# Performance work log

Measured on AMD Instinct MI355X. Metric: run time of the kernel, lower is better.

Reference implementation:

```python
import jax, jax.numpy as jnp
import numpy as np

C, P, PQ, D, B, HW = 32, 64, 4, 2048, 256, 7
N = HW * HW  # 49 spatial positions


def _bn(x, g, b):
    # eval-mode BatchNorm2d with running_mean=0, running_var=1
    s = g / jnp.sqrt(1.0 + 1e-5)
    return x * s[None, :, None, None] + b[None, :, None, None]


def _g1x1(x, w):
    # grouped 1x1 conv: x [B, C*pin, H, W], w [C, pout, pin]
    Bs, _, Hh, Ww = x.shape
    xg = x.reshape(Bs, C, w.shape[2], Hh, Ww)
    y = jnp.einsum('bcihw,coi->bcohw', xg, w)
    return y.reshape(Bs, C * w.shape[1], Hh, Ww)


def setup_inputs() -> dict:
    key = jax.random.key(0)
    ks = iter(jax.random.split(key, 40))
    def rn(shape, s=1.0):
        return jax.random.normal(next(ks), shape, jnp.float32) * s
    inp = {
        'x': rn((B, D, HW, HW)),
        'W1': rn((C * P, D), 0.02), 'g1': 1.0 + rn((C * P,), 0.1), 'b1': rn((C * P,), 0.1),
        'W2': rn((C * P, P, 3, 3), 0.04), 'g2': 1.0 + rn((C * P,), 0.1), 'b2': rn((C * P,), 0.1),
        'Wq': rn((C, PQ, P), 0.1), 'gq': 1.0 + rn((C * PQ,), 0.1), 'bq': rn((C * PQ,), 0.1),
        'Wk': rn((C, PQ, P), 0.1), 'gk': 1.0 + rn((C * PQ,), 0.1), 'bk': rn((C * PQ,), 0.1),
        'Wout': rn((C, PQ, P), 0.1), 'gout': 1.0 + rn((C * PQ,), 0.1), 'bout': rn((C * PQ,), 0.1),
        'Wcr': rn((C, C, PQ), 0.1), 'gcr': 1.0 + rn((C * C,), 0.1), 'bcr': rn((C * C,), 0.1),
        'gcr1': 1.0 + rn((C * PQ,), 0.1), 'bcr1': rn((C * PQ,), 0.1),
        'Wa': rn((C, P, PQ), 0.1), 'ba': rn((C * P,), 0.1),
        'Wb': rn((C, P, PQ), 0.1), 'bb': rn((C * P,), 0.1),
        'W3': rn((D, C * P), 0.02), 'g3': 1.0 + rn((D,), 0.1), 'b3': rn((D,), 0.1),
    }
    return inp


def reference(x, W1, g1, b1, W2, g2, b2, Wq, gq, bq, Wk, gk, bk,
              Wout, gout, bout, Wcr, gcr, bcr, gcr1, bcr1,
              Wa, ba, Wb, bb, W3, g3, b3):
    # stem: 1x1 conv + BN, grouped 3x3 conv + BN
    Xc = _bn(jnp.einsum('bdhw,ed->behw', x, W1), g1, b1)             # [B,2048,7,7]
    Zc = _bn(jax.lax.conv_general_dilated(
        Xc, W2, (1, 1), 'SAME', feature_group_count=C,
        dimension_numbers=('NCHW', 'OIHW', 'NCHW')), g2, b2)         # [B,2048,7,7]

    # channel self-attention: per-group q(1xp_) @ k(p_xN)
    pooled = jnp.mean(Zc, axis=(2, 3), keepdims=True)                # AvgPool2d(7) -> 1x1
    q = _bn(_g1x1(pooled, Wq), gq, bq).reshape(-1, C, PQ)            # [B,c,p_]
    k = _bn(_g1x1(Zc, Wk), gk, bk).reshape(-1, C, PQ, N)             # [B,c,p_,N]
    scores = jnp.einsum('bcp,bcpn->bcn', q, k)                       # [B,c,N]
    # torch Softmax2d on 3D [B,1,N] normalizes dim -3 == batch dim (faithful quirk)
    M = jax.nn.softmax(scores, axis=0)                               # [B,c,N]

    Zg = Zc.reshape(-1, C, P, N)
    zout = jnp.einsum('bcpn,bcn->bcp', Zg, M).reshape(-1, C * P, 1, 1)
    hc = _bn(_g1x1(zout, Wout), gout, bout)                          # [B,128,1,1]

    # channel-relation: A [B,c,c] mixes H [B,c,p_]
    A = jnp.tanh(_bn(_g1x1(hc, Wcr), gcr, bcr)).reshape(-1, C, C)
    A = jnp.swapaxes(A, 1, 2)                                        # chunk/cat transpose
    Hm = hc.reshape(-1, C, PQ)                                       # [B,c,p_]
    mix = jnp.matmul(A, Hm) + Hm                                     # [B,c,p_]
    hc_ = jax.nn.relu(_bn(mix.reshape(-1, C * PQ, 1, 1), gcr1, bcr1)).reshape(-1, C, PQ)

    # broadcast back to spatial via attention maps
    M_ = M / jnp.max(M)
    Mchc = jnp.einsum('bcp,bcn->bcpn', hc_, M_).reshape(-1, C * PQ, HW, HW)

    alpha = _g1x1(Mchc, Wa) + ba[None, :, None, None]                # [B,2048,7,7]
    beta = _g1x1(Mchc, Wb) + bb[None, :, None, None]
    Xc_ = jax.nn.relu(Zc * alpha + beta)
    cm = Zc * Xc_

    OUT = _bn(jnp.einsum('behw,de->bdhw', cm, W3), g3, b3)
    return OUT + x
```

## Files before the change

### kernel.cpp

```cpp
#include <hip/hip_runtime.h>
#include <hip/hip_bf16.h>
#include <stdint.h>

#define DI __device__ __forceinline__

typedef __attribute__((ext_vector_type(8))) short short8;
typedef __attribute__((ext_vector_type(4))) float floatx4;

DI float bf2f(short u) {
  union { unsigned int i; float f; } v;
  v.i = ((unsigned int)(unsigned short)u) << 16;
  return v.f;
}
DI short f2bf(float f) {
  union { float f; unsigned int i; } v; v.f = f;
  unsigned int r = v.i + 0x7FFFu + ((v.i >> 16) & 1u);
  return (short)(r >> 16);
}

DI void gload16(const void* g, void* l) {
  __builtin_amdgcn_global_load_lds(
      (const __attribute__((address_space(1))) void*)g,
      (__attribute__((address_space(3))) void*)l,
      16, 0, 0);
}

__global__ __launch_bounds__(256) void k_cvt(const float* __restrict__ src,
                                             short* __restrict__ dst, int n) {
  int i = blockIdx.x * 256 + threadIdx.x;
  if (i < n) dst[i] = f2bf(src[i]);
}

__global__ __launch_bounds__(256) void k_w2r(const float* __restrict__ W2,
                                             short* __restrict__ W2R) {
  int idx = blockIdx.x * 256 + threadIdx.x;
  if (idx >= 32 * 9 * 64 * 64) return;
  int pi = idx & 63;
  int po = (idx >> 6) & 63;
  int ct = idx >> 12;
  int tap = ct % 9, c = ct / 9;
  W2R[idx] = f2bf(W2[((c * 64 + po) * 64 + pi) * 9 + tap]);
}

__global__ __launch_bounds__(256) void k_xt(const float* __restrict__ x,
                                            short* __restrict__ xT) {
  __shared__ float tile[64 * 49];
  int b = blockIdx.x, dc = blockIdx.y;
  const float* xp = x + ((size_t)b * 2048 + dc * 64) * 49;
  for (int i = threadIdx.x; i < 64 * 49; i += 256) tile[i] = xp[i];
  __syncthreads();
  for (int i = threadIdx.x; i < 64 * 49; i += 256) {
    int n = i >> 6, dl = i & 63;
    xT[((size_t)(b * 49 + n)) * 2048 + dc * 64 + dl] = f2bf(tile[dl * 49 + n]);
  }
}

__global__ __launch_bounds__(512, 4) void k_gemm1(
    const short* __restrict__ xT, const short* __restrict__ W1b,
    const float* __restrict__ g1, const float* __restrict__ b1,
    short* __restrict__ XcPad) {
  __shared__ __attribute__((aligned(16))) short As[4096];
  __shared__ __attribute__((aligned(16))) short Bs[4096];
  const int tid = threadIdx.x;
  const int wave = tid >> 6, lane = tid & 63;
  const int wg = blockIdx.x;
  const int swz = (wg & 7) * 196 + (wg >> 3);
  const int mt = swz >> 4, et = swz & 15;
  const int srow = tid >> 2, schunk = tid & 3;
  const short* asrc = xT + (size_t)(mt * 128 + srow) * 2048 + schunk * 8;
  const short* bsrc = W1b + (size_t)(et * 128 + srow) * 2048 + schunk * 8;
  short* alds = &As[wave * 512];
  short* blds = &Bs[wave * 512];
  const int wr = wave >> 2, wc = wave & 3;
  const int aoff = (wr * 64 + (lane & 15)) * 32 + (lane >> 4) * 8;
  const int boff = (wc * 32 + (lane & 15)) * 32 + (lane >> 4) * 8;
  floatx4 acc[4][2] = {};
#pragma unroll 1
  for (int kt = 0; kt < 64; ++kt) {
    const int ko = kt * 32;
    gload16(asrc + ko, alds);
    gload16(bsrc + ko, blds);
    __syncthreads();
    short8 a[4], b[2];
#pragma unroll
    for (int i = 0; i < 4; ++i) a[i] = *(const short8*)&As[aoff + i * 512];
#pragma unroll
    for (int j = 0; j < 2; ++j) b[j] = *(const short8*)&Bs[boff + j * 512];
#pragma unroll
    for (int i = 0; i < 4; ++i)
#pragma unroll
      for (int j = 0; j < 2; ++j)
        acc[i][j] = __builtin_amdgcn_mfma_f32_16x16x32_bf16(a[i], b[j], acc[i][j], 0, 0, 0);
    __syncthreads();
  }
  const float rs = rsqrtf(1.0f + 1e-5f);
  size_t abase[16];
#pragma unroll
  for (int i = 0; i < 4; ++i)
#pragma unroll
    for (int r = 0; r < 4; ++r) {
      int m = mt * 128 + wr * 64 + i * 16 + (lane >> 4) * 4 + r;
      int bb = m / 49, n = m % 49, h = n / 7, w = n % 7;
      abase[i * 4 + r] = ((size_t)bb * 81 + (h + 1) * 9 + (w + 1)) * 2048;
    }
#pragma unroll
  for (int j = 0; j < 2; ++j) {
    int e = et * 128 + wc * 32 + j * 16 + (lane & 15);
    float s = g1[e] * rs, bo = b1[e];
#pragma unroll
    for (int i = 0; i < 4; ++i)
#pragma unroll
      for (int r = 0; r < 4; ++r)
        XcPad[abase[i * 4 + r] + e] = f2bf(acc[i][j][r] * s + bo);
  }
}

__global__ __launch_bounds__(512, 4) void k_conv(
    const short* __restrict__ XcPad, const short* __restrict__ W2R,
    const float* __restrict__ g2, const float* __restrict__ b2,
    short* __restrict__ ZcT) {
  __shared__ __attribute__((aligned(16))) short As[4096];
  __shared__ __attribute__((aligned(16))) short Bs[2048];
  const int tid = threadIdx.x;
  const int wave = tid >> 6, lane = tid & 63;
  const int wg = blockIdx.x;
  const int swz = (wg & 7) * 392 + (wg >> 3);
  const int mt = swz >> 5, c = swz & 31;
  const int srow = tid >> 2, schunk = tid & 3;
  int m0 = mt * 128 + srow;
  int b0 = m0 / 49, n0 = m0 % 49, h0 = n0 / 7, w0 = n0 % 7;
  const short* abase = XcPad + (size_t)c * 64 + schunk * 8;
  const short* wbase = W2R + (size_t)c * 9 * 4096 + srow * 64 + schunk * 8;
  short* alds = &As[wave * 512];
  short* blds = &Bs[wave * 512];
  const int wr = wave >> 1, wc = wave & 1;
  const int aoff = (wr * 32 + (lane & 15)) * 32 + (lane >> 4) * 8;
  const int boff = (wc * 32 + (lane & 15)) * 32 + (lane >> 4) * 8;
  floatx4 acc[2][2] = {};
#pragma unroll 1
  for (int tap = 0; tap < 9; ++tap) {
    const int dy = tap / 3, dx = tap % 3;
    const size_t r0 = ((size_t)b0 * 81 + (h0 + dy) * 9 + (w0 + dx)) * 2048;
#pragma unroll
    for (int kk = 0; kk < 2; ++kk) {
      gload16(abase + r0 + kk * 32, alds);
      if (wave < 4) gload16(wbase + tap * 4096 + kk * 32, blds);
      __syncthreads();
      short8 a[2], b[2];
#pragma unroll
      for (int i = 0; i < 2; ++i) a[i] = *(const short8*)&As[aoff + i * 512];
#pragma unroll
      for (int j = 0; j < 2; ++j) b[j] = *(const short8*)&Bs[boff + j * 512];
#pragma unroll
      for (int i = 0; i < 2; ++i)
#pragma unroll
        for (int j = 0; j < 2; ++j)
          acc[i][j] = __builtin_amdgcn_mfma_f32_16x16x32_bf16(a[i], b[j], acc[i][j], 0, 0, 0);
      __syncthreads();
    }
  }
  const float rs = rsqrtf(1.0f + 1e-5f);
#pragma unroll
  for (int j = 0; j < 2; ++j) {
    int e = c * 64 + wc * 32 + j * 16 + (lane & 15);
    float s = g2[e] * rs, bo = b2[e];
#pragma unroll
    for (int i = 0; i < 2; ++i)
#pragma unroll
      for (int r = 0; r < 4; ++r) {
        int m = mt * 128 + wr * 32 + i * 16 + (lane >> 4) * 4 + r;
        ZcT[(size_t)m * 2048 + e] = f2bf(acc[i][j][r] * s + bo);
      }
  }
}

__global__ __launch_bounds__(256) void k_scores(
    const short* __restrict__ ZcT, const float* __restrict__ Wq,
    const float* __restrict__ gq, const float* __restrict__ bq,
    const float* __restrict__ Wk, const float* __restrict__ gk,
    const float* __restrict__ bk, float* __restrict__ scores) {
  int b = blockIdx.x, t = threadIdx.x;
  __shared__ float pooled[2048];
  __shared__ float qv[128];
  const float rs = rsqrtf(1.0f + 1e-5f);
  for (int e = t; e < 2048; e += 256) {
    float s = 0.f;
    for (int n = 0; n < 49; ++n) s += bf2f(ZcT[((size_t)(b * 49 + n)) * 2048 + e]);
    pooled[e] = s * (1.0f / 49.0f);
  }
  __syncthreads();
  if (t < 128) {
    int c = t >> 2;
    float s = 0.f;
    for (int pi = 0; pi < 64; ++pi) s += Wq[t * 64 + pi] * pooled[c * 64 + pi];
    qv[t] = s * gq[t] * rs + bq[t];
  }
  __syncthreads();
  for (int idx = t; idx < 1568; idx += 256) {
    int c = idx / 49, n = idx % 49;
    const short8* z = (const short8*)&ZcT[((size_t)(b * 49 + n)) * 2048 + c * 64];
    float acc[4] = {0.f, 0.f, 0.f, 0.f};
#pragma unroll
    for (int p8 = 0; p8 < 8; ++p8) {
      short8 v = z[p8];
#pragma unroll
      for (int j = 0; j < 8; ++j) {
        float zv = bf2f(v[j]);
#pragma unroll
        for (int pq = 0; pq < 4; ++pq)
          acc[pq] += Wk[(c * 4 + pq) * 64 + p8 * 8 + j] * zv;
      }
    }
    float sc = 0.f;
#pragma unroll
    for (int pq = 0; pq < 4; ++pq) {
      float kv = acc[pq] * gk[c * 4 + pq] * rs + bk[c * 4 + pq];
      sc += qv[c * 4 + pq] * kv;
    }
    scores[b * 1568 + idx] = sc;
  }
}

__global__ __launch_bounds__(256) void k_softmax(const float* __restrict__ scores,
                                                 float* __restrict__ Msm,
                                                 unsigned int* __restrict__ maxM) {
  int cn = blockIdx.x, t = threadIdx.x;
  float v = scores[t * 1568 + cn];
  __shared__ float red[4], red2[4];
  float m = v;
#pragma unroll
  for (int o = 1; o < 64; o <<= 1) m = fmaxf(m, __shfl_xor(m, o));
  if ((t & 63) == 0) red[t >> 6] = m;
  __syncthreads();
  m = fmaxf(fmaxf(red[0], red[1]), fmaxf(red[2], red[3]));
  float e = expf(v - m);
  float s = e;
#pragma unroll
  for (int o = 1; o < 64; o <<= 1) s += __shfl_xor(s, o);
  if ((t & 63) == 0) red2[t >> 6] = s;
  __syncthreads();
  s = red2[0] + red2[1] + red2[2] + red2[3];
  Msm[t * 1568 + cn] = e / s;
  if (t == 0) atomicMax(maxM, __float_as_uint(1.0f / s));
}

__global__ __launch_bounds__(256) void k_tail(
    const short* __restrict__ ZcT, const float* __restrict__ Msm,
    const float* __restrict__ Wout, const float* __restrict__ gout,
    const float* __restrict__ bout, const float* __restrict__ Wcr,
    const float* __restrict__ gcr, const float* __restrict__ bcr,
    const float* __restrict__ gcr1, const float* __restrict__ bcr1,
    const float* __restrict__ Wa, const float* __restrict__ Wb,
    float* __restrict__ va, float* __restrict__ vb) {
  int b = blockIdx.x, t = threadIdx.x;
  __shared__ float Mrow[1568];
  __shared__ float zout[2048];
  __shared__ float hcl[128];
  __shared__ float tb[1024];
  __shared__ float hcp[128];
  const float rs = rsqrtf(1.0f + 1e-5f);
  for (int i = t; i < 1568; i += 256) Mrow[i] = Msm[b * 1568 + i];
  __syncthreads();
  for (int e = t; e < 2048; e += 256) {
    int c = e >> 6;
    float s = 0.f;
    for (int n = 0; n < 49; ++n)
      s += bf2f(ZcT[((size_t)(b * 49 + n)) * 2048 + e]) * Mrow[c * 49 + n];
    zout[e] = s;
  }
  __syncthreads();
  if (t < 128) {
    int c = t >> 2;
    float s = 0.f;
    for (int p = 0; p < 64; ++p) s += Wout[t * 64 + p] * zout[c * 64 + p];
    hcl[t] = s * gout[t] * rs + bout[t];
  }
  __syncthreads();
  for (int i = t; i < 1024; i += 256) {
    int c = i >> 5;
    float s = 0.f;
#pragma unroll
    for (int k = 0; k < 4; ++k) s += Wcr[i * 4 + k] * hcl[c * 4 + k];
    tb[i] = tanhf(s * gcr[i] * rs + bcr[i]);
  }
  __syncthreads();
  if (t < 128) {
    int i = t >> 2, pq = t & 3;
    float s = hcl[t];
    for (int j = 0; j < 32; ++j) s += tb[j * 32 + i] * hcl[j * 4 + pq];
    hcp[t] = fmaxf(s * gcr1[t] * rs + bcr1[t], 0.0f);
  }
  __syncthreads();
  for (int e = t; e < 2048; e += 256) {
    int c = e >> 6;
    float sa = 0.f, sb = 0.f;
#pragma unroll
    for (int pq = 0; pq < 4; ++pq) {
      float h = hcp[c * 4 + pq];
      sa += Wa[e * 4 + pq] * h;
      sb += Wb[e * 4 + pq] * h;
    }
    va[b * 2048 + e] = sa;
    vb[b * 2048 + e] = sb;
  }
}

__global__ __launch_bounds__(256) void k_cm(
    const short* __restrict__ ZcT, const float* __restrict__ Msm,
    const unsigned int* __restrict__ maxM, const float* __restrict__ va,
    const float* __restrict__ vb, const float* __restrict__ ba,
    const float* __restrict__ bb, short* __restrict__ cm) {
  int m = blockIdx.x;
  int b = m / 49, n = m % 49;
  __shared__ float Minv[32];
  if (threadIdx.x < 32) {
    float mx = __uint_as_float(*maxM);
    Minv[threadIdx.x] = Msm[b * 1568 + threadIdx.x * 49 + n] / mx;
  }
  __syncthreads();
  const int e0 = threadIdx.x * 8;
  short8 z8 = *(const short8*)&ZcT[(size_t)m * 2048 + e0];
  const float mi = Minv[e0 >> 6];
  short8 o;
#pragma unroll
  for (int j = 0; j < 8; ++j) {
    float zc = bf2f(z8[j]);
    float al = va[b * 2048 + e0 + j] * mi + ba[e0 + j];
    float bt = vb[b * 2048 + e0 + j] * mi + bb[e0 + j];
    float xc = fmaxf(zc * al + bt, 0.0f);
    o[j] = f2bf(zc * xc);
  }
  *(short8*)&cm[(size_t)m * 2048 + e0] = o;
}

__global__ __launch_bounds__(512, 4) void k_gemm2(
    const short* __restrict__ W3b, const short* __restrict__ cm,
    const float* __restrict__ g3, const float* __restrict__ b3,
    const float* __restrict__ x, float* __restrict__ out) {
  __shared__ __attribute__((aligned(16))) short As[4096];
  __shared__ __attribute__((aligned(16))) short Bs[4096];
  const int tid = threadIdx.x;
  const int wave = tid >> 6, lane = tid & 63;
  const int wg = blockIdx.x;
  const int swz = (wg & 7) * 196 + (wg >> 3);
  const int mt = swz >> 4, dt = swz & 15;
  const int srow = tid >> 2, schunk = tid & 3;
  const short* asrc = W3b + (size_t)(dt * 128 + srow) * 2048 + schunk * 8;
  const short* bsrc = cm + (size_t)(mt * 128 + srow) * 2048 + schunk * 8;
  short* alds = &As[wave * 512];
  short* blds = &Bs[wave * 512];
  const int wr = wave >> 2, wc = wave & 3;
  const int aoff = (wr * 64 + (lane & 15)) * 32 + (lane >> 4) * 8;
  const int boff = (wc * 32 + (lane & 15)) * 32 + (lane >> 4) * 8;
  floatx4 acc[4][2] = {};
#pragma unroll 1
  for (int kt = 0; kt < 64; ++kt) {
    const int ko = kt * 32;
    gload16(asrc + ko, alds);
    gload16(bsrc + ko, blds);
    __syncthreads();
    short8 a[4], b[2];
#pragma unroll
    for (int i = 0; i < 4; ++i) a[i] = *(const short8*)&As[aoff + i * 512];
#pragma unroll
    for (int j = 0; j < 2; ++j) b[j] = *(const short8*)&Bs[boff + j * 512];
#pragma unroll
    for (int i = 0; i < 4; ++i)
#pragma unroll
      for (int j = 0; j < 2; ++j)
        acc[i][j] = __builtin_amdgcn_mfma_f32_16x16x32_bf16(a[i], b[j], acc[i][j], 0, 0, 0);
    __syncthreads();
  }
  const float rs = rsqrtf(1.0f + 1e-5f);
  size_t cbb[2];
#pragma unroll
  for (int j = 0; j < 2; ++j) {
    int m = mt * 128 + wc * 32 + j * 16 + (lane & 15);
    int bb = m / 49, n = m % 49;
    cbb[j] = (size_t)bb * (2048 * 49) + n;
  }
#pragma unroll
  for (int i = 0; i < 4; ++i)
#pragma unroll
    for (int r = 0; r < 4; ++r) {
      int d = dt * 128 + wr * 64 + i * 16 + (lane >> 4) * 4 + r;
      float s = g3[d] * rs, bo = b3[d];
      size_t dterm = (size_t)d * 49;
#pragma unroll
      for (int j = 0; j < 2; ++j) {
        size_t adr = cbb[j] + dterm;
        out[adr] = acc[i][j][r] * s + bo + x[adr];
      }
    }
}

extern "C" void kernel_launch(void* const* d_in, const int* in_sizes, int n_in,
                              void* d_out, int out_size, void* d_ws, size_t ws_size,
                              hipStream_t stream) {
  (void)in_sizes; (void)n_in; (void)out_size; (void)ws_size;
  const float* x    = (const float*)d_in[0];
  const float* W1   = (const float*)d_in[1];
  const float* g1   = (const float*)d_in[2];
  const float* b1   = (const float*)d_in[3];
  const float* W2   = (const float*)d_in[4];
  const float* g2   = (const float*)d_in[5];
  const float* b2   = (const float*)d_in[6];
  const float* Wq   = (const float*)d_in[7];
  const float* gq   = (const float*)d_in[8];
  const float* bq   = (const float*)d_in[9];
  const float* Wk   = (const float*)d_in[10];
  const float* gk   = (const float*)d_in[11];
  const float* bk   = (const float*)d_in[12];
  const float* Wout = (const float*)d_in[13];
  const float* gout = (const float*)d_in[14];
  const float* bout = (const float*)d_in[15];
  const float* Wcr  = (const float*)d_in[16];
  const float* gcr  = (const float*)d_in[17];
  const float* bcr  = (const float*)d_in[18];
  const float* gcr1 = (const float*)d_in[19];
  const float* bcr1 = (const float*)d_in[20];
  const float* Wa   = (const float*)d_in[21];
  const float* ba   = (const float*)d_in[22];
  const float* Wb   = (const float*)d_in[23];
  const float* bb   = (const float*)d_in[24];
  const float* W3   = (const float*)d_in[25];
  const float* g3   = (const float*)d_in[26];
  const float* b3   = (const float*)d_in[27];
  float* out = (float*)d_out;

  char* ws = (char*)d_ws;
  short* XcPad  = (short*)(ws + 0);
  short* xT     = (short*)(ws + 84934656);
  short* ZcT    = (short*)(ws + 136314880);
  short* W1b    = (short*)(ws + 187695104);
  short* W3b    = (short*)(ws + 196083712);
  short* W2R    = (short*)(ws + 204472320);
  float* scores = (float*)(ws + 209059840);
  float* Msm    = (float*)(ws + 210665472);
  float* va     = (float*)(ws + 212271104);
  float* vb     = (float*)(ws + 214368256);
  unsigned int* maxM = (unsigned int*)(ws + 216465408);
  short* cm = xT;

  hipMemsetAsync(XcPad, 0, 84934656, stream);
  hipMemsetAsync(maxM, 0, 4, stream);

  k_cvt<<<16384, 256, 0, stream>>>(W1, W1b, 4194304);
  k_cvt<<<16384, 256, 0, stream>>>(W3, W3b, 4194304);
  k_w2r<<<4608, 256, 0, stream>>>(W2, W2R);
  k_xt<<<dim3(256, 32), 256, 0, stream>>>(x, xT);
  k_gemm1<<<1568, 512, 0, stream>>>(xT, W1b, g1, b1, XcPad);
  k_conv<<<3136, 512, 0, stream>>>(XcPad, W2R, g2, b2, ZcT);
  k_scores<<<256, 256, 0, stream>>>(ZcT, Wq, gq, bq, Wk, gk, bk, scores);
  k_softmax<<<1568, 256, 0, stream>>>(scores, Msm, maxM);
  k_tail<<<256, 256, 0, stream>>>(ZcT, Msm, Wout, gout, bout, Wcr, gcr, bcr,
                                  gcr1, bcr1, Wa, Wb, va, vb);
  k_cm<<<12544, 256, 0, stream>>>(ZcT, Msm, maxM, va, vb, ba, bb, cm);
  k_gemm2<<<1568, 512, 0, stream>>>(W3b, cm, g3, b3, x, out);
}
```

Measured before the change: 903.2 us.

## Double-buffer LDS with K=64 tiles and XOR swizzle in GEMM and conv kernels

Rewrites the main loops of gemm1, conv and gemm2 to prefetch the next K tile into a second LDS buffer while computing on the current one, using s_waitcnt vmcnt and raw barriers in place of two __syncthreads per step. The K step doubles to 64, which halves the iteration count, and an XOR swizzle on the global-load column breaks LDS bank conflicts on the MFMA fragment reads. The conv kernel now loads a full 3x3 tap per stage. LDS use per block grows fourfold, which may reduce occupancy under launch_bounds(512,4).

```diff
diff --git a/kernel.cpp b/kernel.cpp
--- a/kernel.cpp
+++ b/kernel.cpp
@@ -59,40 +59,68 @@
     const short* __restrict__ xT, const short* __restrict__ W1b,
     const float* __restrict__ g1, const float* __restrict__ b1,
     short* __restrict__ XcPad) {
-  __shared__ __attribute__((aligned(16))) short As[4096];
-  __shared__ __attribute__((aligned(16))) short Bs[4096];
+  __shared__ __attribute__((aligned(16))) short As[2][8192];
+  __shared__ __attribute__((aligned(16))) short Bs[2][8192];
   const int tid = threadIdx.x;
   const int wave = tid >> 6, lane = tid & 63;
   const int wg = blockIdx.x;
   const int swz = (wg & 7) * 196 + (wg >> 3);
   const int mt = swz >> 4, et = swz & 15;
-  const int srow = tid >> 2, schunk = tid & 3;
-  const short* asrc = xT + (size_t)(mt * 128 + srow) * 2048 + schunk * 8;
-  const short* bsrc = W1b + (size_t)(et * 128 + srow) * 2048 + schunk * 8;
-  short* alds = &As[wave * 512];
-  short* blds = &Bs[wave * 512];
+  const int r8 = tid >> 3, p0 = tid & 7;
+  const int gsw = ((p0 ^ (r8 & 7)) << 3);
+  const short* aR0 = xT + (size_t)(mt * 128 + r8) * 2048 + gsw;
+  const short* aR1 = aR0 + (size_t)64 * 2048;
+  const short* bR0 = W1b + (size_t)(et * 128 + r8) * 2048 + gsw;
+  const short* bR1 = bR0 + (size_t)64 * 2048;
+  const int lo0 = r8 * 64 + p0 * 8;
+  const int lo1 = (r8 + 64) * 64 + p0 * 8;
   const int wr = wave >> 2, wc = wave & 3;
-  const int aoff = (wr * 64 + (lane & 15)) * 32 + (lane >> 4) * 8;
-  const int boff = (wc * 32 + (lane & 15)) * 32 + (lane >> 4) * 8;
+  const int la = lane & 15, q = lane >> 4, l7 = lane & 7;
+  const int cx0 = ((q) ^ l7) << 3;
+  const int cx1 = ((4 + q) ^ l7) << 3;
+  int arow[4], brow[2];
+#pragma unroll
+  for (int i = 0; i < 4; ++i) arow[i] = (wr * 64 + i * 16 + la) * 64;
+#pragma unroll
+  for (int j = 0; j < 2; ++j) brow[j] = (wc * 32 + j * 16 + la) * 64;
   floatx4 acc[4][2] = {};
+  auto STAGE = [&](int buf, int kt) {
+    const int ko = kt * 64;
+    gload16(aR0 + ko, &As[buf][lo0]);
+    gload16(aR1 + ko, &As[buf][lo1]);
+    gload16(bR0 + ko, &Bs[buf][lo0]);
+    gload16(bR1 + ko, &Bs[buf][lo1]);
+  };
+  auto COMPUTE = [&](int buf) {
+#pragma unroll
+    for (int kk = 0; kk < 2; ++kk) {
+      const int cx = kk ? cx1 : cx0;
+      short8 a[4], b[2];
+#pragma unroll
+      for (int i = 0; i < 4; ++i) a[i] = *(const short8*)&As[buf][arow[i] + cx];
+#pragma unroll
+      for (int j = 0; j < 2; ++j) b[j] = *(const short8*)&Bs[buf][brow[j] + cx];
+#pragma unroll
+      for (int i = 0; i < 4; ++i)
+#pragma unroll
+        for (int j = 0; j < 2; ++j)
+          acc[i][j] = __builtin_amdgcn_mfma_f32_16x16x32_bf16(a[i], b[j], acc[i][j], 0, 0, 0);
+    }
+  };
+  STAGE(0, 0);
+  int cur = 0;
 #pragma unroll 1
-  for (int kt = 0; kt < 64; ++kt) {
-    const int ko = kt * 32;
-    gload16(asrc + ko, alds);
-    gload16(bsrc + ko, blds);
-    __syncthreads();
-    short8 a[4], b[2];
-#pragma unroll
-    for (int i = 0; i < 4; ++i) a[i] = *(const short8*)&As[aoff + i * 512];
-#pragma unroll
-    for (int j = 0; j < 2; ++j) b[j] = *(const short8*)&Bs[boff + j * 512];
-#pragma unroll
-    for (int i = 0; i < 4; ++i)
-#pragma unroll
-      for (int j = 0; j < 2; ++j)
-        acc[i][j] = __builtin_amdgcn_mfma_f32_16x16x32_bf16(a[i], b[j], acc[i][j], 0, 0, 0);
-    __syncthreads();
-  }
+  for (int kt = 0; kt < 31; ++kt) {
+    STAGE(cur ^ 1, kt + 1);
+    asm volatile("s_waitcnt vmcnt(4)" ::: "memory");
+    __builtin_amdgcn_s_barrier();
+    COMPUTE(cur);
+    __builtin_amdgcn_s_barrier();
+    cur ^= 1;
+  }
+  asm volatile("s_waitcnt vmcnt(0)" ::: "memory");
+  __builtin_amdgcn_s_barrier();
+  COMPUTE(cur);
   const float rs = rsqrtf(1.0f + 1e-5f);
   size_t abase[16];
 #pragma unroll
@@ -119,46 +147,70 @@
     const short* __restrict__ XcPad, const short* __restrict__ W2R,
     const float* __restrict__ g2, const float* __restrict__ b2,
     short* __restrict__ ZcT) {
-  __shared__ __attribute__((aligned(16))) short As[4096];
-  __shared__ __attribute__((aligned(16))) short Bs[2048];
+  __shared__ __attribute__((aligned(16))) short As[2][8192];
+  __shared__ __attribute__((aligned(16))) short Ws[2][4096];
   const int tid = threadIdx.x;
   const int wave = tid >> 6, lane = tid & 63;
   const int wg = blockIdx.x;
   const int swz = (wg & 7) * 392 + (wg >> 3);
   const int mt = swz >> 5, c = swz & 31;
-  const int srow = tid >> 2, schunk = tid & 3;
-  int m0 = mt * 128 + srow;
+  const int r8 = tid >> 3, p0 = tid & 7;
+  const int gsw = ((p0 ^ (r8 & 7)) << 3);
+  int m0 = mt * 128 + r8;
   int b0 = m0 / 49, n0 = m0 % 49, h0 = n0 / 7, w0 = n0 % 7;
-  const short* abase = XcPad + (size_t)c * 64 + schunk * 8;
-  const short* wbase = W2R + (size_t)c * 9 * 4096 + srow * 64 + schunk * 8;
-  short* alds = &As[wave * 512];
-  short* blds = &Bs[wave * 512];
+  int m1 = m0 + 64;
+  int b1v = m1 / 49, n1 = m1 % 49, h1 = n1 / 7, w1 = n1 % 7;
+  const short* aB0 = XcPad + ((size_t)b0 * 81 + (h0 + 1) * 9 + (w0 + 1)) * 2048 + c * 64 + gsw;
+  const short* aB1 = XcPad + ((size_t)b1v * 81 + (h1 + 1) * 9 + (w1 + 1)) * 2048 + c * 64 + gsw;
+  const short* wB = W2R + (size_t)c * 9 * 4096 + r8 * 64 + gsw;
+  const int lo0 = r8 * 64 + p0 * 8;
+  const int lo1 = (r8 + 64) * 64 + p0 * 8;
   const int wr = wave >> 1, wc = wave & 1;
-  const int aoff = (wr * 32 + (lane & 15)) * 32 + (lane >> 4) * 8;
-  const int boff = (wc * 32 + (lane & 15)) * 32 + (lane >> 4) * 8;
+  const int la = lane & 15, q = lane >> 4, l7 = lane & 7;
+  const int cx0 = ((q) ^ l7) << 3;
+  const int cx1 = ((4 + q) ^ l7) << 3;
+  int arow[2], brow[2];
+#pragma unroll
+  for (int i = 0; i < 2; ++i) arow[i] = (wr * 32 + i * 16 + la) * 64;
+#pragma unroll
+  for (int j = 0; j < 2; ++j) brow[j] = (wc * 32 + j * 16 + la) * 64;
   floatx4 acc[2][2] = {};
-#pragma unroll 1
-  for (int tap = 0; tap < 9; ++tap) {
-    const int dy = tap / 3, dx = tap % 3;
-    const size_t r0 = ((size_t)b0 * 81 + (h0 + dy) * 9 + (w0 + dx)) * 2048;
+  auto STAGE = [&](int buf, int tap) {
+    const int toff = ((tap / 3 - 1) * 9 + (tap % 3 - 1)) * 2048;
+    gload16(aB0 + toff, &As[buf][lo0]);
+    gload16(aB1 + toff, &As[buf][lo1]);
+    gload16(wB + tap * 4096, &Ws[buf][lo0]);
+  };
+  auto COMPUTE = [&](int buf) {
 #pragma unroll
     for (int kk = 0; kk < 2; ++kk) {
-      gload16(abase + r0 + kk * 32, alds);
-      if (wave < 4) gload16(wbase + tap * 4096 + kk * 32, blds);
-      __syncthreads();
+      const int cx = kk ? cx1 : cx0;
       short8 a[2], b[2];
 #pragma unroll
-      for (int i = 0; i < 2; ++i) a[i] = *(const short8*)&As[aoff + i * 512];
-#pragma unroll
-      for (int j = 0; j < 2; ++j) b[j] = *(const short8*)&Bs[boff + j * 512];
+      for (int i = 0; i < 2; ++i) a[i] = *(const short8*)&As[buf][arow[i] + cx];
+#pragma unroll
+      for (int j = 0; j < 2; ++j) b[j] = *(const short8*)&Ws[buf][brow[j] + cx];
 #pragma unroll
       for (int i = 0; i < 2; ++i)
 #pragma unroll
         for (int j = 0; j < 2; ++j)
           acc[i][j] = __builtin_amdgcn_mfma_f32_16x16x32_bf16(a[i], b[j], acc[i][j], 0, 0, 0);
-      __syncthreads();
-    }
-  }
+    }
+  };
+  STAGE(0, 0);
+  int cur = 0;
+#pragma unroll 1
+  for (int tap = 0; tap < 8; ++tap) {
+    STAGE(cur ^ 1, tap + 1);
+    asm volatile("s_waitcnt vmcnt(3)" ::: "memory");
+    __builtin_amdgcn_s_barrier();
+    COMPUTE(cur);
+    __builtin_amdgcn_s_barrier();
+    cur ^= 1;
+  }
+  asm volatile("s_waitcnt vmcnt(0)" ::: "memory");
+  __builtin_amdgcn_s_barrier();
+  COMPUTE(cur);
   const float rs = rsqrtf(1.0f + 1e-5f);
 #pragma unroll
   for (int j = 0; j < 2; ++j) {
@@ -337,40 +389,68 @@
     const short* __restrict__ W3b, const short* __restrict__ cm,
     const float* __restrict__ g3, const float* __restrict__ b3,
     const float* __restrict__ x, float* __restrict__ out) {
-  __shared__ __attribute__((aligned(16))) short As[4096];
-  __shared__ __attribute__((aligned(16))) short Bs[4096];
+  __shared__ __attribute__((aligned(16))) short As[2][8192];
+  __shared__ __attribute__((aligned(16))) short Bs[2][8192];
   const int tid = threadIdx.x;
   const int wave = tid >> 6, lane = tid & 63;
   const int wg = blockIdx.x;
   const int swz = (wg & 7) * 196 + (wg >> 3);
   const int mt = swz >> 4, dt = swz & 15;
-  const int srow = tid >> 2, schunk = tid & 3;
-  const short* asrc = W3b + (size_t)(dt * 128 + srow) * 2048 + schunk * 8;
-  const short* bsrc = cm + (size_t)(mt * 128 + srow) * 2048 + schunk * 8;
-  short* alds = &As[wave * 512];
-  short* blds = &Bs[wave * 512];
+  const int r8 = tid >> 3, p0 = tid & 7;
+  const int gsw = ((p0 ^ (r8 & 7)) << 3);
+  const short* aR0 = W3b + (size_t)(dt * 128 + r8) * 2048 + gsw;
+  const short* aR1 = aR0 + (size_t)64 * 2048;
+  const short* bR0 = cm + (size_t)(mt * 128 + r8) * 2048 + gsw;
+  const short* bR1 = bR0 + (size_t)64 * 2048;
+  const int lo0 = r8 * 64 + p0 * 8;
+  const int lo1 = (r8 + 64) * 64 + p0 * 8;
   const int wr = wave >> 2, wc = wave & 3;
-  const int aoff = (wr * 64 + (lane & 15)) * 32 + (lane >> 4) * 8;
-  const int boff = (wc * 32 + (lane & 15)) * 32 + (lane >> 4) * 8;
+  const int la = lane & 15, q = lane >> 4, l7 = lane & 7;
+  const int cx0 = ((q) ^ l7) << 3;
+  const int cx1 = ((4 + q) ^ l7) << 3;
+  int arow[4], brow[2];
+#pragma unroll
+  for (int i = 0; i < 4; ++i) arow[i] = (wr * 64 + i * 16 + la) * 64;
+#pragma unroll
+  for (int j = 0; j < 2; ++j) brow[j] = (wc * 32 + j * 16 + la) * 64;
   floatx4 acc[4][2] = {};
+  auto STAGE = [&](int buf, int kt) {
+    const int ko = kt * 64;
+    gload16(aR0 + ko, &As[buf][lo0]);
+    gload16(aR1 + ko, &As[buf][lo1]);
+    gload16(bR0 + ko, &Bs[buf][lo0]);
+    gload16(bR1 + ko, &Bs[buf][lo1]);
+  };
+  auto COMPUTE = [&](int buf) {
+#pragma unroll
+    for (int kk = 0; kk < 2; ++kk) {
+      const int cx = kk ? cx1 : cx0;
+      short8 a[4], b[2];
+#pragma unroll
+      for (int i = 0; i < 4; ++i) a[i] = *(const short8*)&As[buf][arow[i] + cx];
+#pragma unroll
+      for (int j = 0; j < 2; ++j) b[j] = *(const short8*)&Bs[buf][brow[j] + cx];
+#pragma unroll
+      for (int i = 0; i < 4; ++i)
+#pragma unroll
+        for (int j = 0; j < 2; ++j)
+          acc[i][j] = __builtin_amdgcn_mfma_f32_16x16x32_bf16(a[i], b[j], acc[i][j], 0, 0, 0);
+    }
+  };
+  STAGE(0, 0);
+  int cur = 0;
 #pragma unroll 1
-  for (int kt = 0; kt < 64; ++kt) {
-    const int ko = kt * 32;
-    gload16(asrc + ko, alds);
-    gload16(bsrc + ko, blds);
-    __syncthreads();
-    short8 a[4], b[2];
-#pragma unroll
-    for (int i = 0; i < 4; ++i) a[i] = *(const short8*)&As[aoff + i * 512];
-#pragma unroll
-    for (int j = 0; j < 2; ++j) b[j] = *(const short8*)&Bs[boff + j * 512];
-#pragma unroll
-    for (int i = 0; i < 4; ++i)
-#pragma unroll
-      for (int j = 0; j < 2; ++j)
-        acc[i][j] = __builtin_amdgcn_mfma_f32_16x16x32_bf16(a[i], b[j], acc[i][j], 0, 0, 0);
-    __syncthreads();
-  }
+  for (int kt = 0; kt < 31; ++kt) {
+    STAGE(cur ^ 1, kt + 1);
+    asm volatile("s_waitcnt vmcnt(4)" ::: "memory");
+    __builtin_amdgcn_s_barrier();
+    COMPUTE(cur);
+    __builtin_amdgcn_s_barrier();
+    cur ^= 1;
+  }
+  asm volatile("s_waitcnt vmcnt(0)" ::: "memory");
+  __builtin_amdgcn_s_barrier();
+  COMPUTE(cur);
   const float rs = rsqrtf(1.0f + 1e-5f);
   size_t cbb[2];
 #pragma unroll
```

Result: faster. 850.7 us (-5.8%).
